# Kernel optimization log

Hardware: AMD Instinct MI355X
Metric: run time of the kernel (lower is better)

Reference implementation:

```python
import jax, jax.numpy as jnp
import numpy as np

B, S, D0, D, H = 8, 1024, 128, 256, 8
HD = D // H  # head_dim = 32


def setup_inputs() -> dict:
    key = jax.random.key(0)
    k0, k1, k2, k3, k4, k5 = jax.random.split(key, 6)
    query = jax.random.normal(k0, (B, S, D0), dtype=jnp.float32)
    U = jax.random.normal(k1, (B, H, S, S), dtype=jnp.float32)
    # nn.Linear(in, out, bias=False) weights have shape (out, in)
    sc = 1.0 / np.sqrt(D0)
    Wq = jax.random.normal(k2, (D, D0), dtype=jnp.float32) * sc
    Wk = jax.random.normal(k3, (D, D0), dtype=jnp.float32) * sc
    Wv = jax.random.normal(k4, (D, D0), dtype=jnp.float32) * sc
    Wo = jax.random.normal(k5, (D0, D), dtype=jnp.float32) * (1.0 / np.sqrt(D))
    return {"query": query, "U": U, "Wq": Wq, "Wk": Wk, "Wv": Wv, "Wo": Wo}


def reference(query, U, Wq, Wk, Wv, Wo):
    b, s, _ = query.shape
    # projections: y = x @ W.T ; split heads -> (B, H, S, HD)
    def proj(W):
        y = jnp.einsum('bsd,ed->bse', query, W)
        return y.reshape(b, s, H, HD).transpose(0, 2, 1, 3)

    Q, K, V = proj(Wq), proj(Wk), proj(Wv)
    scale = jnp.sqrt(jnp.asarray(HD, dtype=jnp.float32))
    scores = (jnp.einsum('bhqd,bhkd->bhqk', Q, K) + U) / scale  # (B,H,S,S)
    # mask computed from Q (as in original): key positions where Q rows sum to 0
    mask = (Q.sum(axis=-1) != 0)[:, :, None, :]  # (B,H,1,S), broadcasts over queries
    scores = jnp.where(mask, scores, -jnp.inf)
    attn = jax.nn.softmax(scores, axis=-1)
    out = jnp.einsum('bhqk,bhkd->bhqd', attn, V)  # (B,H,S,HD)
    out = out.transpose(0, 2, 1, 3).reshape(b, s, H * HD)
    output = jnp.einsum('bse,oe->bso', out, Wo)  # (B,S,D0)
    return output, attn
```

## Files before the change

kernel.cpp:

```cpp
#include <hip/hip_runtime.h>
#include <stdint.h>
#include <math.h>

#define B_ 8
#define S_ 1024
#define D0_ 128
#define D_ 256
#define H_ 8
#define HD_ 32
#define BH_ (B_*H_)

typedef __attribute__((ext_vector_type(8))) short short8;
typedef __attribute__((ext_vector_type(4))) float f32x4;
typedef __attribute__((ext_vector_type(4))) unsigned int u32x4;
typedef __attribute__((ext_vector_type(2))) float f32x2;

__device__ __forceinline__ unsigned short f2bf(float x) {
    unsigned int u = __float_as_uint(x);
    u += 0x7FFFu + ((u >> 16) & 1u);
    return (unsigned short)(u >> 16);
}
__device__ __forceinline__ float bf2f(unsigned short s) {
    return __uint_as_float(((unsigned int)s) << 16);
}

__global__ __launch_bounds__(256) void proj_kernel(
    const float* __restrict__ query,
    const float* __restrict__ Wq, const float* __restrict__ Wk, const float* __restrict__ Wv,
    unsigned short* __restrict__ Qhi, unsigned short* __restrict__ Qlo,
    unsigned short* __restrict__ Khi, unsigned short* __restrict__ Klo,
    unsigned short* __restrict__ Vt, float* __restrict__ maskbias)
{
    const int z = blockIdx.z;
    const float* W = (z == 0) ? Wq : (z == 1) ? Wk : Wv;
    const int m0 = blockIdx.x * 64;
    const int n0 = blockIdx.y * 64;
    __shared__ float xs[64 * 68];
    __shared__ float ws[64 * 68];
    __shared__ float msum[64][2];
    const int t = threadIdx.x;
    const int ty = t >> 4, tx = t & 15;
    if (z == 0 && t < 128) msum[t >> 1][t & 1] = 0.f;
    float acc[4][4] = {};
    for (int kc = 0; kc < 128; kc += 64) {
        #pragma unroll
        for (int it = 0; it < 4; ++it) {
            int fi = t + it * 256;
            int row = fi >> 4, c4 = fi & 15;
            *(float4*)(&xs[row * 68 + c4 * 4]) = *(const float4*)(&query[(size_t)(m0 + row) * 128 + kc + c4 * 4]);
            *(float4*)(&ws[row * 68 + c4 * 4]) = *(const float4*)(&W[(size_t)(n0 + row) * 128 + kc + c4 * 4]);
        }
        __syncthreads();
        #pragma unroll
        for (int k4 = 0; k4 < 16; ++k4) {
            float4 a4[4], b4[4];
            #pragma unroll
            for (int i = 0; i < 4; ++i) a4[i] = *(const float4*)(&xs[(ty * 4 + i) * 68 + k4 * 4]);
            #pragma unroll
            for (int j = 0; j < 4; ++j) b4[j] = *(const float4*)(&ws[(tx * 4 + j) * 68 + k4 * 4]);
            #pragma unroll
            for (int i = 0; i < 4; ++i)
                #pragma unroll
                for (int j = 0; j < 4; ++j)
                    acc[i][j] += a4[i].x * b4[j].x + a4[i].y * b4[j].y + a4[i].z * b4[j].z + a4[i].w * b4[j].w;
        }
        __syncthreads();
    }
    #pragma unroll
    for (int i = 0; i < 4; ++i) {
        int m = m0 + ty * 4 + i;
        int b = m >> 10, s = m & 1023;
        #pragma unroll
        for (int j = 0; j < 4; ++j) {
            int o = n0 + tx * 4 + j;
            int h = o >> 5, d = o & 31;
            int bh = b * 8 + h;
            float y = acc[i][j];
            if (z < 2) {
                unsigned short hi = f2bf(y);
                unsigned short lo = f2bf(y - bf2f(hi));
                size_t idx = ((size_t)(bh * 1024 + s)) * 32 + d;
                if (z == 0) { Qhi[idx] = hi; Qlo[idx] = lo; }
                else        { Khi[idx] = hi; Klo[idx] = lo; }
            } else {
                Vt[((size_t)(bh * 32 + d)) * 1024 + s] = f2bf(y);
            }
        }
    }
    if (z == 0) {
        #pragma unroll
        for (int i = 0; i < 4; ++i) {
            float ps = acc[i][0] + acc[i][1] + acc[i][2] + acc[i][3];
            atomicAdd(&msum[ty * 4 + i][tx >> 3], ps);
        }
        __syncthreads();
        if (t < 128) {
            int row = t >> 1, hh = t & 1;
            int m = m0 + row;
            int b = m >> 10, s = m & 1023;
            int bh = b * 8 + (n0 >> 5) + hh;
            maskbias[bh * 1024 + s] = (msum[row][hh] != 0.0f) ? 0.0f : -INFINITY;
        }
    }
}

__global__ __launch_bounds__(256, 4) void attn_kernel(
    const unsigned short* __restrict__ Qhi, const unsigned short* __restrict__ Qlo,
    const unsigned short* __restrict__ Khi, const unsigned short* __restrict__ Klo,
    const unsigned short* __restrict__ Vt, const float* __restrict__ maskbias,
    const float* __restrict__ U, float* __restrict__ attn_out, float* __restrict__ out_buf)
{
    __shared__ float Ored[4 * 16 * 36];
    __shared__ float redMS[4][2][16];

    const int bid = blockIdx.x;
    const int swz = (bid & 7) * 512 + (bid >> 3);
    const int bh = swz >> 6;
    const int qbase = (swz & 63) << 4;
    const int tid = threadIdx.x;
    const int wid = tid >> 6;
    const int c = tid & 15;
    const int g = (tid >> 4) & 3;
    const int kstrip = wid << 8;

    const size_t bh_qk = (size_t)bh * S_ * 32;
    const size_t bh_u = (size_t)bh * S_ * S_;
    const int q = qbase + c;

    const float* Urow = U + bh_u + (size_t)q * S_;
    f32x4 s[16];
    #pragma unroll
    for (int kf = 0; kf < 16; ++kf)
        s[kf] = *(const f32x4*)(Urow + kstrip + kf * 16 + g * 4);

    short8 qh = *(const short8*)(Qhi + bh_qk + (size_t)q * 32 + 8 * g);
    short8 ql = *(const short8*)(Qlo + bh_qk + (size_t)q * 32 + 8 * g);

    #pragma unroll
    for (int kf = 0; kf < 16; ++kf) {
        size_t koff = bh_qk + (size_t)(kstrip + kf * 16 + c) * 32 + 8 * g;
        short8 kh = *(const short8*)(Khi + koff);
        short8 kl = *(const short8*)(Klo + koff);
        s[kf] = __builtin_amdgcn_mfma_f32_16x16x32_bf16(kh, qh, s[kf], 0, 0, 0);
        s[kf] = __builtin_amdgcn_mfma_f32_16x16x32_bf16(kl, qh, s[kf], 0, 0, 0);
        s[kf] = __builtin_amdgcn_mfma_f32_16x16x32_bf16(kh, ql, s[kf], 0, 0, 0);
    }

    const float inv_scale = 0.17677669529663687f;
    const float* mbrow = maskbias + bh * S_;
    #pragma unroll
    for (int kf = 0; kf < 16; ++kf) {
        int k0 = kstrip + kf * 16 + g * 4;
        f32x4 mb = *(const f32x4*)(mbrow + k0);
        #pragma unroll
        for (int r = 0; r < 4; ++r)
            s[kf][r] = s[kf][r] * inv_scale + mb[r];
    }

    float m = s[0][0];
    #pragma unroll
    for (int kf = 0; kf < 16; ++kf)
        #pragma unroll
        for (int r = 0; r < 4; ++r) m = fmaxf(m, s[kf][r]);
    m = fmaxf(m, __shfl_xor(m, 16, 64));
    m = fmaxf(m, __shfl_xor(m, 32, 64));
    m = fmaxf(m, -1e30f);

    float sum = 0.f;
    #pragma unroll
    for (int kf = 0; kf < 16; ++kf)
        #pragma unroll
        for (int r = 0; r < 4; ++r) {
            float p = __expf(s[kf][r] - m);
            s[kf][r] = p;
            sum += p;
        }
    sum += __shfl_xor(sum, 16, 64);
    sum += __shfl_xor(sum, 32, 64);
    if (g == 0) { redMS[wid][0][c] = m; redMS[wid][1][c] = sum; }
    __syncthreads();

    float m0 = redMS[0][0][c], m1 = redMS[1][0][c], m2 = redMS[2][0][c], m3 = redMS[3][0][c];
    float M = fmaxf(fmaxf(m0, m1), fmaxf(m2, m3));
    float S = redMS[0][1][c] * __expf(m0 - M) + redMS[1][1][c] * __expf(m1 - M)
            + redMS[2][1][c] * __expf(m2 - M) + redMS[3][1][c] * __expf(m3 - M);
    const float fw = __expf(m - M) / S;

    const int srcA = c + 32 * (g & 1);
    const int srcB = srcA + 16;
    const int gd2 = g >> 1;
    f32x4 o0 = (f32x4){0.f, 0.f, 0.f, 0.f};
    f32x4 o1 = (f32x4){0.f, 0.f, 0.f, 0.f};
    const unsigned short* vb0 = Vt + (size_t)(bh * 32 + c) * 1024 + kstrip;
    const unsigned short* vb1 = vb0 + 16 * 1024;
    #pragma unroll
    for (int ch = 0; ch < 8; ++ch) {
        unsigned int p0[2], p1[2];
        p0[0] = __builtin_amdgcn_perm(__float_as_uint(s[2 * ch][1]), __float_as_uint(s[2 * ch][0]), 0x07060302u);
        p0[1] = __builtin_amdgcn_perm(__float_as_uint(s[2 * ch][3]), __float_as_uint(s[2 * ch][2]), 0x07060302u);
        p1[0] = __builtin_amdgcn_perm(__float_as_uint(s[2 * ch + 1][1]), __float_as_uint(s[2 * ch + 1][0]), 0x07060302u);
        p1[1] = __builtin_amdgcn_perm(__float_as_uint(s[2 * ch + 1][3]), __float_as_uint(s[2 * ch + 1][2]), 0x07060302u);
        unsigned int b0A = (unsigned int)__shfl((int)p0[0], srcA, 64);
        unsigned int b1A = (unsigned int)__shfl((int)p0[1], srcA, 64);
        unsigned int b0B = (unsigned int)__shfl((int)p0[0], srcB, 64);
        unsigned int b1B = (unsigned int)__shfl((int)p0[1], srcB, 64);
        unsigned int c0A = (unsigned int)__shfl((int)p1[0], srcA, 64);
        unsigned int c1A = (unsigned int)__shfl((int)p1[1], srcA, 64);
        unsigned int c0B = (unsigned int)__shfl((int)p1[0], srcB, 64);
        unsigned int c1B = (unsigned int)__shfl((int)p1[1], srcB, 64);
        union { u32x4 u; short8 h; } bb;
        bb.u[0] = gd2 ? c0A : b0A;
        bb.u[1] = gd2 ? c1A : b1A;
        bb.u[2] = gd2 ? c0B : b0B;
        bb.u[3] = gd2 ? c1B : b1B;
        short8 A0 = *(const short8*)(vb0 + ch * 32 + g * 8);
        short8 A1 = *(const short8*)(vb1 + ch * 32 + g * 8);
        o0 = __builtin_amdgcn_mfma_f32_16x16x32_bf16(A0, bb.h, o0, 0, 0, 0);
        o1 = __builtin_amdgcn_mfma_f32_16x16x32_bf16(A1, bb.h, o1, 0, 0, 0);
    }
    #pragma unroll
    for (int r = 0; r < 4; ++r) { o0[r] *= fw; o1[r] *= fw; }
    *(f32x4*)(&Ored[(wid * 16 + c) * 36 + g * 4]) = o0;
    *(f32x4*)(&Ored[(wid * 16 + c) * 36 + 16 + g * 4]) = o1;
    __syncthreads();

    const int qq = tid >> 4;
    const int dd = (tid & 15) * 2;
    float v0 = 0.f, v1 = 0.f;
    #pragma unroll
    for (int w = 0; w < 4; ++w) {
        v0 += Ored[(w * 16 + qq) * 36 + dd];
        v1 += Ored[(w * 16 + qq) * 36 + dd + 1];
    }
    const int b = bh >> 3, h = bh & 7;
    f32x2 vv = {v0, v1};
    *(f32x2*)(out_buf + ((size_t)(b * 1024 + qbase + qq)) * 256 + h * 32 + dd) = vv;

    float* arow = attn_out + bh_u + (size_t)q * S_;
    #pragma unroll
    for (int kf = 0; kf < 16; ++kf) {
        int k0 = kstrip + kf * 16 + g * 4;
        f32x4 a;
        #pragma unroll
        for (int r = 0; r < 4; ++r) a[r] = s[kf][r] * fw;
        *(f32x4*)(arow + k0) = a;
    }
}

__global__ __launch_bounds__(256) void outproj_kernel(
    const float* __restrict__ xb, const float* __restrict__ Wo, float* __restrict__ outp)
{
    const int m0 = blockIdx.x * 64;
    const int n0 = blockIdx.y * 64;
    __shared__ float xs[64 * 68];
    __shared__ float ws[64 * 68];
    const int t = threadIdx.x;
    const int ty = t >> 4, tx = t & 15;
    float acc[4][4] = {};
    for (int kc = 0; kc < 256; kc += 64) {
        #pragma unroll
        for (int it = 0; it < 4; ++it) {
            int fi = t + it * 256;
            int row = fi >> 4, c4 = fi & 15;
            *(float4*)(&xs[row * 68 + c4 * 4]) = *(const float4*)(&xb[(size_t)(m0 + row) * 256 + kc + c4 * 4]);
            *(float4*)(&ws[row * 68 + c4 * 4]) = *(const float4*)(&Wo[(size_t)(n0 + row) * 256 + kc + c4 * 4]);
        }
        __syncthreads();
        #pragma unroll
        for (int k4 = 0; k4 < 16; ++k4) {
            float4 a4[4], b4[4];
            #pragma unroll
            for (int i = 0; i < 4; ++i) a4[i] = *(const float4*)(&xs[(ty * 4 + i) * 68 + k4 * 4]);
            #pragma unroll
            for (int j = 0; j < 4; ++j) b4[j] = *(const float4*)(&ws[(tx * 4 + j) * 68 + k4 * 4]);
            #pragma unroll
            for (int i = 0; i < 4; ++i)
                #pragma unroll
                for (int j = 0; j < 4; ++j)
                    acc[i][j] += a4[i].x * b4[j].x + a4[i].y * b4[j].y + a4[i].z * b4[j].z + a4[i].w * b4[j].w;
        }
        __syncthreads();
    }
    #pragma unroll
    for (int i = 0; i < 4; ++i)
        #pragma unroll
        for (int j = 0; j < 4; ++j)
            outp[(size_t)(m0 + ty * 4 + i) * 128 + n0 + tx * 4 + j] = acc[i][j];
}

extern "C" void kernel_launch(void* const* d_in, const int* in_sizes, int n_in,
                              void* d_out, int out_size, void* d_ws, size_t ws_size,
                              hipStream_t stream)
{
    const float* query = (const float*)d_in[0];
    const float* U     = (const float*)d_in[1];
    const float* Wq    = (const float*)d_in[2];
    const float* Wk    = (const float*)d_in[3];
    const float* Wv    = (const float*)d_in[4];
    const float* Wo    = (const float*)d_in[5];

    float* output = (float*)d_out;
    float* attn   = (float*)d_out + (size_t)B_ * S_ * D0_;

    const size_t NQK = (size_t)BH_ * S_ * 32;
    unsigned short* Qhi = (unsigned short*)d_ws;
    unsigned short* Qlo = Qhi + NQK;
    unsigned short* Khi = Qlo + NQK;
    unsigned short* Klo = Khi + NQK;
    unsigned short* Vt  = Klo + NQK;
    float* maskbias = (float*)(Vt + NQK);
    float* out_buf  = maskbias + (size_t)BH_ * S_;

    proj_kernel<<<dim3(128, 4, 3), 256, 0, stream>>>(query, Wq, Wk, Wv, Qhi, Qlo, Khi, Klo, Vt, maskbias);
    attn_kernel<<<dim3(4096), 256, 0, stream>>>(Qhi, Qlo, Khi, Klo, Vt, maskbias, U, attn, out_buf);
    outproj_kernel<<<dim3(128, 2), 256, 0, stream>>>(out_buf, Wo, output);
}
```

Baseline: 259.4 us.

## Stage U tile into LDS via async global_load_lds overlapping QK MFMAs

```diff
diff --git a/kernel.cpp b/kernel.cpp
--- a/kernel.cpp
+++ b/kernel.cpp
@@ -14,6 +14,13 @@
 typedef __attribute__((ext_vector_type(4))) float f32x4;
 typedef __attribute__((ext_vector_type(4))) unsigned int u32x4;
 typedef __attribute__((ext_vector_type(2))) float f32x2;
+
+typedef __attribute__((address_space(3))) unsigned int lds_u32;
+typedef __attribute__((address_space(1))) const unsigned int glb_u32;
+
+__device__ __forceinline__ void lds_stage16(void* lds, const void* g) {
+    __builtin_amdgcn_global_load_lds((glb_u32*)g, (lds_u32*)lds, 16, 0, 0);
+}
 
 __device__ __forceinline__ unsigned short f2bf(float x) {
     unsigned int u = __float_as_uint(x);
@@ -104,14 +111,17 @@
     }
 }
 
-__global__ __launch_bounds__(256, 4) void attn_kernel(
+#define ATTN_LDS (65536 + 9216 + 512)
+__global__ __launch_bounds__(256, 2) void attn_kernel(
     const unsigned short* __restrict__ Qhi, const unsigned short* __restrict__ Qlo,
     const unsigned short* __restrict__ Khi, const unsigned short* __restrict__ Klo,
     const unsigned short* __restrict__ Vt, const float* __restrict__ maskbias,
     const float* __restrict__ U, float* __restrict__ attn_out, float* __restrict__ out_buf)
 {
-    __shared__ float Ored[4 * 16 * 36];
-    __shared__ float redMS[4][2][16];
+    extern __shared__ char lds_raw[];
+    float* Ulds = (float*)lds_raw;
+    float* Ored = (float*)(lds_raw + 65536);
+    float* redMS = (float*)(lds_raw + 65536 + 9216);
 
     const int bid = blockIdx.x;
     const int swz = (bid & 7) * 512 + (bid >> 3);
@@ -119,6 +129,7 @@
     const int qbase = (swz & 63) << 4;
     const int tid = threadIdx.x;
     const int wid = tid >> 6;
+    const int lane = tid & 63;
     const int c = tid & 15;
     const int g = (tid >> 4) & 3;
     const int kstrip = wid << 8;
@@ -127,14 +138,22 @@
     const size_t bh_u = (size_t)bh * S_ * S_;
     const int q = qbase + c;
 
-    const float* Urow = U + bh_u + (size_t)q * S_;
-    f32x4 s[16];
-    #pragma unroll
-    for (int kf = 0; kf < 16; ++kf)
-        s[kf] = *(const f32x4*)(Urow + kstrip + kf * 16 + g * 4);
+    {
+        const float* gbase = U + bh_u + (size_t)qbase * S_ + kstrip;
+        float* lbase = Ulds + wid * 4096;
+        #pragma unroll
+        for (int cp = 0; cp < 16; ++cp) {
+            const float* gsrc = gbase + (size_t)cp * S_ + (((lane + cp) & 63) << 2);
+            lds_stage16(lbase + cp * 256, gsrc);
+        }
+    }
 
     short8 qh = *(const short8*)(Qhi + bh_qk + (size_t)q * 32 + 8 * g);
     short8 ql = *(const short8*)(Qlo + bh_qk + (size_t)q * 32 + 8 * g);
+
+    f32x4 s[16];
+    #pragma unroll
+    for (int kf = 0; kf < 16; ++kf) s[kf] = (f32x4){0.f, 0.f, 0.f, 0.f};
 
     #pragma unroll
     for (int kf = 0; kf < 16; ++kf) {
@@ -146,15 +165,20 @@
         s[kf] = __builtin_amdgcn_mfma_f32_16x16x32_bf16(kh, ql, s[kf], 0, 0, 0);
     }
 
+    asm volatile("s_waitcnt vmcnt(0)" ::: "memory");
+    __builtin_amdgcn_sched_barrier(0);
+
     const float inv_scale = 0.17677669529663687f;
     const float* mbrow = maskbias + bh * S_;
+    const float* myU = Ulds + wid * 4096 + c * 256;
     #pragma unroll
     for (int kf = 0; kf < 16; ++kf) {
         int k0 = kstrip + kf * 16 + g * 4;
+        f32x4 u = *(const f32x4*)(myU + (((kf * 4 + g - c) & 63) << 2));
         f32x4 mb = *(const f32x4*)(mbrow + k0);
         #pragma unroll
         for (int r = 0; r < 4; ++r)
-            s[kf][r] = s[kf][r] * inv_scale + mb[r];
+            s[kf][r] = (s[kf][r] + u[r]) * inv_scale + mb[r];
     }
 
     float m = s[0][0];
@@ -177,13 +201,13 @@
         }
     sum += __shfl_xor(sum, 16, 64);
     sum += __shfl_xor(sum, 32, 64);
-    if (g == 0) { redMS[wid][0][c] = m; redMS[wid][1][c] = sum; }
+    if (g == 0) { redMS[wid * 32 + c] = m; redMS[wid * 32 + 16 + c] = sum; }
     __syncthreads();
 
-    float m0 = redMS[0][0][c], m1 = redMS[1][0][c], m2 = redMS[2][0][c], m3 = redMS[3][0][c];
+    float m0 = redMS[0 * 32 + c], m1 = redMS[1 * 32 + c], m2 = redMS[2 * 32 + c], m3 = redMS[3 * 32 + c];
     float M = fmaxf(fmaxf(m0, m1), fmaxf(m2, m3));
-    float S = redMS[0][1][c] * __expf(m0 - M) + redMS[1][1][c] * __expf(m1 - M)
-            + redMS[2][1][c] * __expf(m2 - M) + redMS[3][1][c] * __expf(m3 - M);
+    float S = redMS[0 * 32 + 16 + c] * __expf(m0 - M) + redMS[1 * 32 + 16 + c] * __expf(m1 - M)
+            + redMS[2 * 32 + 16 + c] * __expf(m2 - M) + redMS[3 * 32 + 16 + c] * __expf(m3 - M);
     const float fw = __expf(m - M) / S;
 
     const int srcA = c + 32 * (g & 1);
@@ -312,6 +336,10 @@
     float* out_buf  = maskbias + (size_t)BH_ * S_;
 
     proj_kernel<<<dim3(128, 4, 3), 256, 0, stream>>>(query, Wq, Wk, Wv, Qhi, Qlo, Khi, Klo, Vt, maskbias);
-    attn_kernel<<<dim3(4096), 256, 0, stream>>>(Qhi, Qlo, Khi, Klo, Vt, maskbias, U, attn, out_buf);
+
+    hipFuncSetAttribute(reinterpret_cast<const void*>(attn_kernel),
+                        hipFuncAttributeMaxDynamicSharedMemorySize, ATTN_LDS);
+    attn_kernel<<<dim3(4096), 256, ATTN_LDS, stream>>>(Qhi, Qlo, Khi, Klo, Vt, maskbias, U, attn, out_buf);
+
     outproj_kernel<<<dim3(128, 2), 256, 0, stream>>>(out_buf, Wo, output);
 }
```

Result: slower. 282.4 us (+8.9%).

## Stage U tiles through LDS via global_load_lds and coalesce attn stores

Applied to the files above, without the earlier changes.

```diff
diff --git a/kernel.cpp b/kernel.cpp
--- a/kernel.cpp
+++ b/kernel.cpp
@@ -14,6 +14,13 @@
 typedef __attribute__((ext_vector_type(4))) float f32x4;
 typedef __attribute__((ext_vector_type(4))) unsigned int u32x4;
 typedef __attribute__((ext_vector_type(2))) float f32x2;
+
+typedef __attribute__((address_space(3))) unsigned int lds_u32;
+typedef __attribute__((address_space(1))) const unsigned int glb_u32;
+
+__device__ __forceinline__ void lds_stage16(void* lds, const void* g) {
+    __builtin_amdgcn_global_load_lds((glb_u32*)g, (lds_u32*)lds, 16, 0, 0);
+}
 
 __device__ __forceinline__ unsigned short f2bf(float x) {
     unsigned int u = __float_as_uint(x);
@@ -110,6 +117,7 @@
     const unsigned short* __restrict__ Vt, const float* __restrict__ maskbias,
     const float* __restrict__ U, float* __restrict__ attn_out, float* __restrict__ out_buf)
 {
+    __shared__ float Ubuf[4 * 2048];
     __shared__ float Ored[4 * 16 * 36];
     __shared__ float redMS[4][2][16];
 
@@ -119,6 +127,7 @@
     const int qbase = (swz & 63) << 4;
     const int tid = threadIdx.x;
     const int wid = tid >> 6;
+    const int lane = tid & 63;
     const int c = tid & 15;
     const int g = (tid >> 4) & 3;
     const int kstrip = wid << 8;
@@ -127,17 +136,26 @@
     const size_t bh_u = (size_t)bh * S_ * S_;
     const int q = qbase + c;
 
-    const float* Urow = U + bh_u + (size_t)q * S_;
-    f32x4 s[16];
-    #pragma unroll
-    for (int kf = 0; kf < 16; ++kf)
-        s[kf] = *(const f32x4*)(Urow + kstrip + kf * 16 + g * 4);
+    float* wU = Ubuf + wid * 2048;
+    const int l5 = lane >> 5;
+    const int s32 = lane & 31;
+    const float* Ug = U + bh_u + (size_t)qbase * S_ + kstrip;
+
+    #pragma unroll
+    for (int i = 0; i < 8; ++i) {
+        int row = 2 * i + l5;
+        lds_stage16(wU + i * 256, Ug + (size_t)row * S_ + 4 * (s32 ^ (row & 7)));
+    }
 
     short8 qh = *(const short8*)(Qhi + bh_qk + (size_t)q * 32 + 8 * g);
     short8 ql = *(const short8*)(Qlo + bh_qk + (size_t)q * 32 + 8 * g);
 
-    #pragma unroll
-    for (int kf = 0; kf < 16; ++kf) {
+    f32x4 s[16];
+    #pragma unroll
+    for (int kf = 0; kf < 16; ++kf) s[kf] = (f32x4){0.f, 0.f, 0.f, 0.f};
+
+    #pragma unroll
+    for (int kf = 0; kf < 8; ++kf) {
         size_t koff = bh_qk + (size_t)(kstrip + kf * 16 + c) * 32 + 8 * g;
         short8 kh = *(const short8*)(Khi + koff);
         short8 kl = *(const short8*)(Klo + koff);
@@ -146,12 +164,50 @@
         s[kf] = __builtin_amdgcn_mfma_f32_16x16x32_bf16(kh, ql, s[kf], 0, 0, 0);
     }
 
+    asm volatile("s_waitcnt vmcnt(0)" ::: "memory");
+    __builtin_amdgcn_sched_barrier(0);
+
+    #pragma unroll
+    for (int kf = 0; kf < 8; ++kf) {
+        f32x4 u = *(const f32x4*)(wU + c * 128 + 4 * ((4 * kf + g) ^ (c & 7)));
+        #pragma unroll
+        for (int r = 0; r < 4; ++r) s[kf][r] += u[r];
+    }
+    asm volatile("s_waitcnt lgkmcnt(0)" ::: "memory");
+    __builtin_amdgcn_sched_barrier(0);
+
+    #pragma unroll
+    for (int i = 0; i < 8; ++i) {
+        int row = 2 * i + l5;
+        lds_stage16(wU + i * 256, Ug + (size_t)row * S_ + 128 + 4 * (s32 ^ (row & 7)));
+    }
+    __builtin_amdgcn_sched_barrier(0);
+
+    #pragma unroll
+    for (int kf = 8; kf < 16; ++kf) {
+        size_t koff = bh_qk + (size_t)(kstrip + kf * 16 + c) * 32 + 8 * g;
+        short8 kh = *(const short8*)(Khi + koff);
+        short8 kl = *(const short8*)(Klo + koff);
+        s[kf] = __builtin_amdgcn_mfma_f32_16x16x32_bf16(kh, qh, s[kf], 0, 0, 0);
+        s[kf] = __builtin_amdgcn_mfma_f32_16x16x32_bf16(kl, qh, s[kf], 0, 0, 0);
+        s[kf] = __builtin_amdgcn_mfma_f32_16x16x32_bf16(kh, ql, s[kf], 0, 0, 0);
+    }
+
+    asm volatile("s_waitcnt vmcnt(0)" ::: "memory");
+    __builtin_amdgcn_sched_barrier(0);
+
+    #pragma unroll
+    for (int kf = 8; kf < 16; ++kf) {
+        f32x4 u = *(const f32x4*)(wU + c * 128 + 4 * ((4 * (kf - 8) + g) ^ (c & 7)));
+        #pragma unroll
+        for (int r = 0; r < 4; ++r) s[kf][r] += u[r];
+    }
+
     const float inv_scale = 0.17677669529663687f;
     const float* mbrow = maskbias + bh * S_;
     #pragma unroll
     for (int kf = 0; kf < 16; ++kf) {
-        int k0 = kstrip + kf * 16 + g * 4;
-        f32x4 mb = *(const f32x4*)(mbrow + k0);
+        f32x4 mb = *(const f32x4*)(mbrow + kstrip + kf * 16 + g * 4);
         #pragma unroll
         for (int r = 0; r < 4; ++r)
             s[kf][r] = s[kf][r] * inv_scale + mb[r];
@@ -236,14 +292,31 @@
     f32x2 vv = {v0, v1};
     *(f32x2*)(out_buf + ((size_t)(b * 1024 + qbase + qq)) * 256 + h * 32 + dd) = vv;
 
-    float* arow = attn_out + bh_u + (size_t)q * S_;
-    #pragma unroll
-    for (int kf = 0; kf < 16; ++kf) {
-        int k0 = kstrip + kf * 16 + g * 4;
-        f32x4 a;
-        #pragma unroll
-        for (int r = 0; r < 4; ++r) a[r] = s[kf][r] * fw;
-        *(f32x4*)(arow + k0) = a;
+    asm volatile("s_waitcnt lgkmcnt(0)" ::: "memory");
+    __builtin_amdgcn_sched_barrier(0);
+    #pragma unroll
+    for (int hh = 0; hh < 2; ++hh) {
+        #pragma unroll
+        for (int kf8 = 0; kf8 < 8; ++kf8) {
+            const int kf = hh * 8 + kf8;
+            f32x4 a;
+            #pragma unroll
+            for (int r = 0; r < 4; ++r) a[r] = s[kf][r] * fw;
+            *(f32x4*)(wU + c * 128 + 4 * ((4 * kf8 + g) ^ (c & 7))) = a;
+        }
+        asm volatile("s_waitcnt lgkmcnt(0)" ::: "memory");
+        __builtin_amdgcn_sched_barrier(0);
+        #pragma unroll
+        for (int i = 0; i < 8; ++i) {
+            int row = 2 * i + l5;
+            f32x4 v = *(const f32x4*)(wU + row * 128 + 4 * s32);
+            int j = s32 ^ (row & 7);
+            *(f32x4*)(attn_out + bh_u + (size_t)(qbase + row) * S_ + kstrip + 128 * hh + 4 * j) = v;
+        }
+        if (hh == 0) {
+            asm volatile("s_waitcnt lgkmcnt(0)" ::: "memory");
+            __builtin_amdgcn_sched_barrier(0);
+        }
     }
 }
 
```

Measured after the change: 268.6 us. +3.5%, slower.

## Use split-bf16 MFMA for projection and output-projection GEMMs

Applied to the files above, without the earlier changes.

```diff
diff --git a/kernel.cpp b/kernel.cpp
--- a/kernel.cpp
+++ b/kernel.cpp
@@ -14,6 +14,7 @@
 typedef __attribute__((ext_vector_type(4))) float f32x4;
 typedef __attribute__((ext_vector_type(4))) unsigned int u32x4;
 typedef __attribute__((ext_vector_type(2))) float f32x2;
+typedef __attribute__((ext_vector_type(4))) unsigned short u16x4;
 
 __device__ __forceinline__ unsigned short f2bf(float x) {
     unsigned int u = __float_as_uint(x);
@@ -22,6 +23,18 @@
 }
 __device__ __forceinline__ float bf2f(unsigned short s) {
     return __uint_as_float(((unsigned int)s) << 16);
+}
+__device__ __forceinline__ void split_hi_lo(f32x4 a, f32x4 b, short8& hi, short8& lo) {
+    #pragma unroll
+    for (int i = 0; i < 4; ++i) {
+        unsigned short h = f2bf(a[i]);
+        hi[i] = (short)h; lo[i] = (short)f2bf(a[i] - bf2f(h));
+    }
+    #pragma unroll
+    for (int i = 0; i < 4; ++i) {
+        unsigned short h = f2bf(b[i]);
+        hi[4 + i] = (short)h; lo[4 + i] = (short)f2bf(b[i] - bf2f(h));
+    }
 }
 
 __global__ __launch_bounds__(256) void proj_kernel(
@@ -33,72 +46,95 @@
 {
     const int z = blockIdx.z;
     const float* W = (z == 0) ? Wq : (z == 1) ? Wk : Wv;
-    const int m0 = blockIdx.x * 64;
-    const int n0 = blockIdx.y * 64;
-    __shared__ float xs[64 * 68];
-    __shared__ float ws[64 * 68];
+    const int bm = blockIdx.x * 64;
+    const int bn = blockIdx.y * 64;
     __shared__ float msum[64][2];
-    const int t = threadIdx.x;
-    const int ty = t >> 4, tx = t & 15;
-    if (z == 0 && t < 128) msum[t >> 1][t & 1] = 0.f;
-    float acc[4][4] = {};
-    for (int kc = 0; kc < 128; kc += 64) {
-        #pragma unroll
-        for (int it = 0; it < 4; ++it) {
-            int fi = t + it * 256;
-            int row = fi >> 4, c4 = fi & 15;
-            *(float4*)(&xs[row * 68 + c4 * 4]) = *(const float4*)(&query[(size_t)(m0 + row) * 128 + kc + c4 * 4]);
-            *(float4*)(&ws[row * 68 + c4 * 4]) = *(const float4*)(&W[(size_t)(n0 + row) * 128 + kc + c4 * 4]);
-        }
+    const int tid = threadIdx.x;
+    const int wid = tid >> 6;
+    const int c = tid & 15;
+    const int g = (tid >> 4) & 3;
+
+    if (z == 0) {
+        if (tid < 128) msum[tid >> 1][tid & 1] = 0.f;
         __syncthreads();
-        #pragma unroll
-        for (int k4 = 0; k4 < 16; ++k4) {
-            float4 a4[4], b4[4];
+    }
+
+    const int mrow = bm + wid * 16 + c;
+    short8 xh[4], xl[4];
+    #pragma unroll
+    for (int kk = 0; kk < 4; ++kk) {
+        f32x4 a = *(const f32x4*)(query + (size_t)mrow * 128 + kk * 32 + 8 * g);
+        f32x4 b = *(const f32x4*)(query + (size_t)mrow * 128 + kk * 32 + 8 * g + 4);
+        split_hi_lo(a, b, xh[kk], xl[kk]);
+    }
+
+    float ph0 = 0.f, ph1 = 0.f;
+    #pragma unroll
+    for (int nt = 0; nt < 4; ++nt) {
+        const int nrow = bn + nt * 16 + c;
+        short8 wh[4], wl[4];
+        #pragma unroll
+        for (int kk = 0; kk < 4; ++kk) {
+            f32x4 a = *(const f32x4*)(W + (size_t)nrow * 128 + kk * 32 + 8 * g);
+            f32x4 b = *(const f32x4*)(W + (size_t)nrow * 128 + kk * 32 + 8 * g + 4);
+            split_hi_lo(a, b, wh[kk], wl[kk]);
+        }
+        f32x4 acc = (f32x4){0.f, 0.f, 0.f, 0.f};
+        if (z < 2) {
             #pragma unroll
-            for (int i = 0; i < 4; ++i) a4[i] = *(const float4*)(&xs[(ty * 4 + i) * 68 + k4 * 4]);
+            for (int kk = 0; kk < 4; ++kk) {
+                acc = __builtin_amdgcn_mfma_f32_16x16x32_bf16(wh[kk], xh[kk], acc, 0, 0, 0);
+                acc = __builtin_amdgcn_mfma_f32_16x16x32_bf16(wl[kk], xh[kk], acc, 0, 0, 0);
+                acc = __builtin_amdgcn_mfma_f32_16x16x32_bf16(wh[kk], xl[kk], acc, 0, 0, 0);
+            }
+            const int b_ = mrow >> 10, s = mrow & 1023;
+            const int n0 = bn + nt * 16 + g * 4;
+            const int h = n0 >> 5, d0 = n0 & 31;
+            const int bh = b_ * 8 + h;
+            u16x4 h4, l4;
             #pragma unroll
-            for (int j = 0; j < 4; ++j) b4[j] = *(const float4*)(&ws[(tx * 4 + j) * 68 + k4 * 4]);
+            for (int r = 0; r < 4; ++r) {
+                unsigned short hh = f2bf(acc[r]);
+                h4[r] = hh;
+                l4[r] = f2bf(acc[r] - bf2f(hh));
+            }
+            size_t idx = ((size_t)(bh * 1024 + s)) * 32 + d0;
+            if (z == 0) {
+                *(u16x4*)(Qhi + idx) = h4;
+                *(u16x4*)(Qlo + idx) = l4;
+                float psum = acc[0] + acc[1] + acc[2] + acc[3];
+                if (nt < 2) ph0 += psum; else ph1 += psum;
+            } else {
+                *(u16x4*)(Khi + idx) = h4;
+                *(u16x4*)(Klo + idx) = l4;
+            }
+        } else {
             #pragma unroll
-            for (int i = 0; i < 4; ++i)
-                #pragma unroll
-                for (int j = 0; j < 4; ++j)
-                    acc[i][j] += a4[i].x * b4[j].x + a4[i].y * b4[j].y + a4[i].z * b4[j].z + a4[i].w * b4[j].w;
-        }
+            for (int kk = 0; kk < 4; ++kk) {
+                acc = __builtin_amdgcn_mfma_f32_16x16x32_bf16(xh[kk], wh[kk], acc, 0, 0, 0);
+                acc = __builtin_amdgcn_mfma_f32_16x16x32_bf16(xl[kk], wh[kk], acc, 0, 0, 0);
+                acc = __builtin_amdgcn_mfma_f32_16x16x32_bf16(xh[kk], wl[kk], acc, 0, 0, 0);
+            }
+            const int m0 = bm + wid * 16 + g * 4;
+            const int b_ = m0 >> 10, s0 = m0 & 1023;
+            const int n = bn + nt * 16 + c;
+            const int h = n >> 5, d = n & 31;
+            const int bh = b_ * 8 + h;
+            u16x4 v4;
+            #pragma unroll
+            for (int r = 0; r < 4; ++r) v4[r] = f2bf(acc[r]);
+            *(u16x4*)(Vt + ((size_t)(bh * 32 + d)) * 1024 + s0) = v4;
+        }
+    }
+    if (z == 0) {
+        atomicAdd(&msum[wid * 16 + c][0], ph0);
+        atomicAdd(&msum[wid * 16 + c][1], ph1);
         __syncthreads();
-    }
-    #pragma unroll
-    for (int i = 0; i < 4; ++i) {
-        int m = m0 + ty * 4 + i;
-        int b = m >> 10, s = m & 1023;
-        #pragma unroll
-        for (int j = 0; j < 4; ++j) {
-            int o = n0 + tx * 4 + j;
-            int h = o >> 5, d = o & 31;
-            int bh = b * 8 + h;
-            float y = acc[i][j];
-            if (z < 2) {
-                unsigned short hi = f2bf(y);
-                unsigned short lo = f2bf(y - bf2f(hi));
-                size_t idx = ((size_t)(bh * 1024 + s)) * 32 + d;
-                if (z == 0) { Qhi[idx] = hi; Qlo[idx] = lo; }
-                else        { Khi[idx] = hi; Klo[idx] = lo; }
-            } else {
-                Vt[((size_t)(bh * 32 + d)) * 1024 + s] = f2bf(y);
-            }
-        }
-    }
-    if (z == 0) {
-        #pragma unroll
-        for (int i = 0; i < 4; ++i) {
-            float ps = acc[i][0] + acc[i][1] + acc[i][2] + acc[i][3];
-            atomicAdd(&msum[ty * 4 + i][tx >> 3], ps);
-        }
-        __syncthreads();
-        if (t < 128) {
-            int row = t >> 1, hh = t & 1;
-            int m = m0 + row;
-            int b = m >> 10, s = m & 1023;
-            int bh = b * 8 + (n0 >> 5) + hh;
+        if (tid < 128) {
+            int row = tid >> 1, hh = tid & 1;
+            int m = bm + row;
+            int b_ = m >> 10, s = m & 1023;
+            int bh = b_ * 8 + (bn >> 5) + hh;
             maskbias[bh * 1024 + s] = (msum[row][hh] != 0.0f) ? 0.0f : -INFINITY;
         }
     }
@@ -250,42 +286,35 @@
 __global__ __launch_bounds__(256) void outproj_kernel(
     const float* __restrict__ xb, const float* __restrict__ Wo, float* __restrict__ outp)
 {
-    const int m0 = blockIdx.x * 64;
-    const int n0 = blockIdx.y * 64;
-    __shared__ float xs[64 * 68];
-    __shared__ float ws[64 * 68];
-    const int t = threadIdx.x;
-    const int ty = t >> 4, tx = t & 15;
-    float acc[4][4] = {};
-    for (int kc = 0; kc < 256; kc += 64) {
-        #pragma unroll
-        for (int it = 0; it < 4; ++it) {
-            int fi = t + it * 256;
-            int row = fi >> 4, c4 = fi & 15;
-            *(float4*)(&xs[row * 68 + c4 * 4]) = *(const float4*)(&xb[(size_t)(m0 + row) * 256 + kc + c4 * 4]);
-            *(float4*)(&ws[row * 68 + c4 * 4]) = *(const float4*)(&Wo[(size_t)(n0 + row) * 256 + kc + c4 * 4]);
-        }
-        __syncthreads();
-        #pragma unroll
-        for (int k4 = 0; k4 < 16; ++k4) {
-            float4 a4[4], b4[4];
-            #pragma unroll
-            for (int i = 0; i < 4; ++i) a4[i] = *(const float4*)(&xs[(ty * 4 + i) * 68 + k4 * 4]);
-            #pragma unroll
-            for (int j = 0; j < 4; ++j) b4[j] = *(const float4*)(&ws[(tx * 4 + j) * 68 + k4 * 4]);
-            #pragma unroll
-            for (int i = 0; i < 4; ++i)
-                #pragma unroll
-                for (int j = 0; j < 4; ++j)
-                    acc[i][j] += a4[i].x * b4[j].x + a4[i].y * b4[j].y + a4[i].z * b4[j].z + a4[i].w * b4[j].w;
-        }
-        __syncthreads();
-    }
-    #pragma unroll
-    for (int i = 0; i < 4; ++i)
-        #pragma unroll
-        for (int j = 0; j < 4; ++j)
-            outp[(size_t)(m0 + ty * 4 + i) * 128 + n0 + tx * 4 + j] = acc[i][j];
+    const int bm = blockIdx.x * 64;
+    const int bn = blockIdx.y * 64;
+    const int tid = threadIdx.x;
+    const int wid = tid >> 6, c = tid & 15, g = (tid >> 4) & 3;
+    const int mrow = bm + wid * 16 + c;
+
+    short8 xh[8], xl[8];
+    #pragma unroll
+    for (int kk = 0; kk < 8; ++kk) {
+        f32x4 a = *(const f32x4*)(xb + (size_t)mrow * 256 + kk * 32 + 8 * g);
+        f32x4 b = *(const f32x4*)(xb + (size_t)mrow * 256 + kk * 32 + 8 * g + 4);
+        split_hi_lo(a, b, xh[kk], xl[kk]);
+    }
+    #pragma unroll
+    for (int nt = 0; nt < 4; ++nt) {
+        const int nrow = bn + nt * 16 + c;
+        f32x4 acc = (f32x4){0.f, 0.f, 0.f, 0.f};
+        #pragma unroll
+        for (int kk = 0; kk < 8; ++kk) {
+            f32x4 a = *(const f32x4*)(Wo + (size_t)nrow * 256 + kk * 32 + 8 * g);
+            f32x4 b = *(const f32x4*)(Wo + (size_t)nrow * 256 + kk * 32 + 8 * g + 4);
+            short8 wh, wl;
+            split_hi_lo(a, b, wh, wl);
+            acc = __builtin_amdgcn_mfma_f32_16x16x32_bf16(wh, xh[kk], acc, 0, 0, 0);
+            acc = __builtin_amdgcn_mfma_f32_16x16x32_bf16(wl, xh[kk], acc, 0, 0, 0);
+            acc = __builtin_amdgcn_mfma_f32_16x16x32_bf16(wh, xl[kk], acc, 0, 0, 0);
+        }
+        *(f32x4*)(outp + (size_t)mrow * 128 + bn + nt * 16 + g * 4) = acc;
+    }
 }
 
 extern "C" void kernel_launch(void* const* d_in, const int* in_sizes, int n_in,
```

Result: faster. 219.1 us, median of 2 (-15.5%).
